# Optimization experiments

Measured on AMD Instinct MI355X. Metric: run time of the kernel, lower is better.

The kernel has to match this reference:

```python
import jax, jax.numpy as jnp
import numpy as np

M, K, N, E = 8192, 1024, 1024, 8  # total tokens, in-dim, out-dim, experts/segments


def setup_inputs() -> dict:
    key = jax.random.key(0)
    k1, k2, k3 = jax.random.split(key, 3)
    a = jax.random.normal(k1, (M, K), dtype=jnp.float32)
    b = jax.random.normal(k2, (E, N, K), dtype=jnp.float32) * 0.02  # column-major per-expert weights
    c = jnp.zeros((M, N), dtype=jnp.float32)
    inner = jnp.sort(jax.random.randint(k3, (E - 1,), 0, M, dtype=jnp.int32))
    seg_indptr = jnp.concatenate([
        jnp.zeros((1,), jnp.int32), inner, jnp.full((1,), M, jnp.int32)
    ])  # [E+1], monotone, covers [0, M)
    weight_indices = jnp.arange(E, dtype=jnp.int32)
    return {
        "a": a, "b": b, "c": c,
        "batch_size": E, "weight_column_major": 1,
        "seg_indptr": seg_indptr, "weight_indices": weight_indices,
    }


def reference(a, b, c, batch_size, weight_column_major, seg_indptr, weight_indices):
    # Grouped GEMM: for each contiguous segment s of rows [seg_indptr[s], seg_indptr[s+1]),
    # c[rows] = a[rows] @ b[weight_indices[s]].T  (b is [E, N, K], column-major weights).
    assert weight_column_major
    rows = jnp.arange(a.shape[0])[:, None]  # [M, 1]
    out = c
    for s in range(batch_size):  # fixed small loop over experts/segments
        b_e = jnp.take(b, weight_indices[s], axis=0)  # [N, K]
        seg_out = a @ b_e.T                            # [M, N]
        mask = (rows >= seg_indptr[s]) & (rows < seg_indptr[s + 1])
        out = jnp.where(mask, seg_out, out)
    return out
```

## Files before the change

kernel.cpp:

```cpp
#include <hip/hip_runtime.h>
#include <hip/hip_bf16.h>

#define MDIM 8192
#define KDIM 1024
#define NDIM 1024
#define NEXP 8
#define BM 128
#define BN 128
#define BK 32
#define LDSS 40

typedef __attribute__((ext_vector_type(8))) short bf16x8;
typedef __attribute__((ext_vector_type(4))) float floatx4;

static __device__ __forceinline__ unsigned short f2b(float f) {
    unsigned int u = __float_as_uint(f);
    return (unsigned short)((u + 0x7fffu + ((u >> 16) & 1u)) >> 16);
}

static __device__ __forceinline__ void cvt_store4(unsigned short* dst, float4 v) {
    ushort4 u;
    u.x = f2b(v.x); u.y = f2b(v.y); u.z = f2b(v.z); u.w = f2b(v.w);
    *reinterpret_cast<ushort4*>(dst) = u;
}

__global__ __launch_bounds__(256, 2)
void grouped_gemm_bf16(const float* __restrict__ a,
                       const float* __restrict__ b,
                       const int* __restrict__ seg_indptr,
                       const int* __restrict__ widx,
                       float* __restrict__ c)
{
    __shared__ unsigned short As[BM * LDSS];
    __shared__ unsigned short Bs[BN * LDSS];

    const int NTN = NDIM / BN;
    int rem = (int)blockIdx.x;
    int s = -1, m0 = 0, seg_end = 0, n0 = 0;
    for (int i = 0; i < NEXP; ++i) {
        int ps = seg_indptr[i], pe = seg_indptr[i + 1];
        int nt = ((pe - ps + BM - 1) / BM) * NTN;
        if (rem < nt) {
            s = i; m0 = ps + (rem / NTN) * BM; n0 = (rem % NTN) * BN; seg_end = pe;
            break;
        }
        rem -= nt;
    }
    if (s < 0) return;

    const float* __restrict__ be = b + (size_t)widx[s] * (size_t)(NDIM * KDIM);

    const int tid = (int)threadIdx.x;
    const int r0 = tid >> 3;
    const int kc = (tid & 7) * 4;

    int arow[4];
#pragma unroll
    for (int u = 0; u < 4; ++u) {
        int r = m0 + r0 + 32 * u;
        arow[u] = r < MDIM ? r : MDIM - 1;
    }

    const int lane = tid & 63;
    const int wave = tid >> 6;
    const int wm = (wave & 1) * 64;
    const int wn = (wave >> 1) * 64;
    const int fr = lane & 15;
    const int quad = lane >> 4;

    floatx4 acc[4][4] = {};

    float4 av[4], bv[4];
#pragma unroll
    for (int u = 0; u < 4; ++u) {
        av[u] = *reinterpret_cast<const float4*>(a + (size_t)arow[u] * KDIM + kc);
        bv[u] = *reinterpret_cast<const float4*>(be + (size_t)(n0 + r0 + 32 * u) * KDIM + kc);
    }

    for (int k0 = 0; k0 < KDIM; k0 += BK) {
        __syncthreads();
#pragma unroll
        for (int u = 0; u < 4; ++u) {
            cvt_store4(&As[(r0 + 32 * u) * LDSS + kc], av[u]);
            cvt_store4(&Bs[(r0 + 32 * u) * LDSS + kc], bv[u]);
        }
        const int kn = (k0 + BK < KDIM) ? (k0 + BK) : 0;
#pragma unroll
        for (int u = 0; u < 4; ++u) {
            av[u] = *reinterpret_cast<const float4*>(a + (size_t)arow[u] * KDIM + kn + kc);
            bv[u] = *reinterpret_cast<const float4*>(be + (size_t)(n0 + r0 + 32 * u) * KDIM + kn + kc);
        }
        __syncthreads();

        bf16x8 af[4], bf[4];
#pragma unroll
        for (int mi = 0; mi < 4; ++mi)
            af[mi] = *reinterpret_cast<const bf16x8*>(&As[(wm + mi * 16 + fr) * LDSS + quad * 8]);
#pragma unroll
        for (int ni = 0; ni < 4; ++ni)
            bf[ni] = *reinterpret_cast<const bf16x8*>(&Bs[(wn + ni * 16 + fr) * LDSS + quad * 8]);
#pragma unroll
        for (int mi = 0; mi < 4; ++mi)
#pragma unroll
            for (int ni = 0; ni < 4; ++ni)
                acc[mi][ni] = __builtin_amdgcn_mfma_f32_16x16x32_bf16(af[mi], bf[ni], acc[mi][ni], 0, 0, 0);
    }

#pragma unroll
    for (int mi = 0; mi < 4; ++mi) {
        const int rbase = m0 + wm + mi * 16 + quad * 4;
#pragma unroll
        for (int ni = 0; ni < 4; ++ni) {
            const int col = n0 + wn + ni * 16 + fr;
#pragma unroll
            for (int j = 0; j < 4; ++j) {
                const int row = rbase + j;
                if (row < seg_end)
                    c[(size_t)row * NDIM + col] = acc[mi][ni][j];
            }
        }
    }
}

extern "C" void kernel_launch(void* const* d_in, const int* in_sizes, int n_in,
                              void* d_out, int out_size, void* d_ws, size_t ws_size,
                              hipStream_t stream) {
    const float* a          = (const float*)d_in[0];
    const float* b          = (const float*)d_in[1];
    const int*   seg_indptr = (const int*)d_in[5];
    const int*   widx       = (const int*)d_in[6];
    float*       out        = (float*)d_out;

    dim3 grid(568), block(256);
    hipLaunchKernelGGL(grouped_gemm_bf16, grid, block, 0, stream,
                       a, b, seg_indptr, widx, out);
}
```

Baseline: 174.2 us.

## Pre-convert inputs to bf16 in workspace and stream tiles via global_load_lds

Adds a separate conversion kernel that casts A and all expert weights to bf16 into the workspace. The GEMM then reads half-width data and copies tiles straight into LDS with global_load_lds, removing per-tile in-register conversion and the register staging round trip. In exchange it pays an extra full read and write pass over A and B plus a second launch. It also drops the register prefetch and LDS padding, which can expose load latency and bank conflicts. The old fused kernel is kept as a fallback when the workspace is too small.

```diff
diff --git a/kernel.cpp b/kernel.cpp
--- a/kernel.cpp
+++ b/kernel.cpp
@@ -1,5 +1,6 @@
 #include <hip/hip_runtime.h>
 #include <hip/hip_bf16.h>
+#include <stdint.h>
 
 #define MDIM 8192
 #define KDIM 1024
@@ -12,27 +13,43 @@
 
 typedef __attribute__((ext_vector_type(8))) short bf16x8;
 typedef __attribute__((ext_vector_type(4))) float floatx4;
+typedef __attribute__((ext_vector_type(8))) unsigned short ushort8;
 
 static __device__ __forceinline__ unsigned short f2b(float f) {
     unsigned int u = __float_as_uint(f);
     return (unsigned short)((u + 0x7fffu + ((u >> 16) & 1u)) >> 16);
 }
 
-static __device__ __forceinline__ void cvt_store4(unsigned short* dst, float4 v) {
-    ushort4 u;
-    u.x = f2b(v.x); u.y = f2b(v.y); u.z = f2b(v.z); u.w = f2b(v.w);
-    *reinterpret_cast<ushort4*>(dst) = u;
-}
+__global__ __launch_bounds__(256)
+void cvt_bf16(const float* __restrict__ a, const float* __restrict__ b,
+              unsigned short* __restrict__ wa, unsigned short* __restrict__ wb)
+{
+    const long t  = (long)blockIdx.x * 256 + threadIdx.x;
+    const long NA = (long)MDIM * KDIM / 8;
+    const float* src; unsigned short* dst; long v;
+    if (t < NA) { src = a; dst = wa; v = t; }
+    else        { src = b; dst = wb; v = t - NA; }
+    const float4 lo = ((const float4*)src)[2 * v];
+    const float4 hi = ((const float4*)src)[2 * v + 1];
+    ushort8 o;
+    o[0] = f2b(lo.x); o[1] = f2b(lo.y); o[2] = f2b(lo.z); o[3] = f2b(lo.w);
+    o[4] = f2b(hi.x); o[5] = f2b(hi.y); o[6] = f2b(hi.z); o[7] = f2b(hi.w);
+    ((ushort8*)dst)[v] = o;
+}
+
+#define GLDS(gp, lp) __builtin_amdgcn_global_load_lds(                        \
+    (const __attribute__((address_space(1))) unsigned int*)(gp),              \
+    (__attribute__((address_space(3))) unsigned int*)(lp), 16, 0, 0)
 
 __global__ __launch_bounds__(256, 2)
-void grouped_gemm_bf16(const float* __restrict__ a,
-                       const float* __restrict__ b,
-                       const int* __restrict__ seg_indptr,
-                       const int* __restrict__ widx,
-                       float* __restrict__ c)
+void grouped_gemm_ws(const unsigned short* __restrict__ A,
+                     const unsigned short* __restrict__ B,
+                     const int* __restrict__ seg_indptr,
+                     const int* __restrict__ widx,
+                     float* __restrict__ c)
 {
-    __shared__ unsigned short As[BM * LDSS];
-    __shared__ unsigned short Bs[BN * LDSS];
+    __shared__ unsigned short As[BM * BK];
+    __shared__ unsigned short Bs[BN * BK];
 
     const int NTN = NDIM / BN;
     int rem = (int)blockIdx.x;
@@ -40,49 +57,122 @@
     for (int i = 0; i < NEXP; ++i) {
         int ps = seg_indptr[i], pe = seg_indptr[i + 1];
         int nt = ((pe - ps + BM - 1) / BM) * NTN;
-        if (rem < nt) {
-            s = i; m0 = ps + (rem / NTN) * BM; n0 = (rem % NTN) * BN; seg_end = pe;
-            break;
-        }
+        if (rem < nt) { s = i; m0 = ps + (rem / NTN) * BM; n0 = (rem % NTN) * BN; seg_end = pe; break; }
         rem -= nt;
     }
     if (s < 0) return;
 
+    const unsigned short* __restrict__ be = B + (size_t)widx[s] * (size_t)(NDIM * KDIM);
+
+    const int tid  = (int)threadIdx.x;
+    const int wave = tid >> 6;
+    const int lane = tid & 63;
+    const int srow = tid >> 2;
+    const int skc  = (tid & 3) * 8;
+    int arow0 = m0 + srow;       if (arow0 >= MDIM) arow0 = MDIM - 1;
+    int arow1 = m0 + 64 + srow;  if (arow1 >= MDIM) arow1 = MDIM - 1;
+    const int brow0 = n0 + srow, brow1 = n0 + 64 + srow;
+    const int ldsoff = wave * 16 * BK;
+
+    const int wm = (wave & 1) * 64;
+    const int wn = (wave >> 1) * 64;
+    const int fr = lane & 15;
+    const int quad = lane >> 4;
+
+    floatx4 acc[4][4] = {};
+
+    const unsigned short* aptr0 = A  + (size_t)arow0 * KDIM + skc;
+    const unsigned short* aptr1 = A  + (size_t)arow1 * KDIM + skc;
+    const unsigned short* bptr0 = be + (size_t)brow0 * KDIM + skc;
+    const unsigned short* bptr1 = be + (size_t)brow1 * KDIM + skc;
+
+    for (int k0 = 0; k0 < KDIM; k0 += BK) {
+        GLDS(aptr0 + k0, &As[ldsoff]);
+        GLDS(aptr1 + k0, &As[64 * BK + ldsoff]);
+        GLDS(bptr0 + k0, &Bs[ldsoff]);
+        GLDS(bptr1 + k0, &Bs[64 * BK + ldsoff]);
+        __syncthreads();
+
+        bf16x8 af[4], bf[4];
+#pragma unroll
+        for (int mi = 0; mi < 4; ++mi)
+            af[mi] = *reinterpret_cast<const bf16x8*>(&As[(wm + mi * 16 + fr) * BK + quad * 8]);
+#pragma unroll
+        for (int ni = 0; ni < 4; ++ni)
+            bf[ni] = *reinterpret_cast<const bf16x8*>(&Bs[(wn + ni * 16 + fr) * BK + quad * 8]);
+#pragma unroll
+        for (int mi = 0; mi < 4; ++mi)
+#pragma unroll
+            for (int ni = 0; ni < 4; ++ni)
+                acc[mi][ni] = __builtin_amdgcn_mfma_f32_16x16x32_bf16(af[mi], bf[ni], acc[mi][ni], 0, 0, 0);
+        __syncthreads();
+    }
+
+#pragma unroll
+    for (int mi = 0; mi < 4; ++mi) {
+        const int rbase = m0 + wm + mi * 16 + quad * 4;
+#pragma unroll
+        for (int ni = 0; ni < 4; ++ni) {
+            const int col = n0 + wn + ni * 16 + fr;
+#pragma unroll
+            for (int j = 0; j < 4; ++j) {
+                const int row = rbase + j;
+                if (row < seg_end)
+                    c[(size_t)row * NDIM + col] = acc[mi][ni][j];
+            }
+        }
+    }
+}
+
+__global__ __launch_bounds__(256, 2)
+void grouped_gemm_fused(const float* __restrict__ a, const float* __restrict__ b,
+                        const int* __restrict__ seg_indptr, const int* __restrict__ widx,
+                        float* __restrict__ c)
+{
+    __shared__ unsigned short As[BM * LDSS];
+    __shared__ unsigned short Bs[BN * LDSS];
+    const int NTN = NDIM / BN;
+    int rem = (int)blockIdx.x;
+    int s = -1, m0 = 0, seg_end = 0, n0 = 0;
+    for (int i = 0; i < NEXP; ++i) {
+        int ps = seg_indptr[i], pe = seg_indptr[i + 1];
+        int nt = ((pe - ps + BM - 1) / BM) * NTN;
+        if (rem < nt) { s = i; m0 = ps + (rem / NTN) * BM; n0 = (rem % NTN) * BN; seg_end = pe; break; }
+        rem -= nt;
+    }
+    if (s < 0) return;
     const float* __restrict__ be = b + (size_t)widx[s] * (size_t)(NDIM * KDIM);
-
     const int tid = (int)threadIdx.x;
     const int r0 = tid >> 3;
     const int kc = (tid & 7) * 4;
-
     int arow[4];
 #pragma unroll
     for (int u = 0; u < 4; ++u) {
         int r = m0 + r0 + 32 * u;
         arow[u] = r < MDIM ? r : MDIM - 1;
     }
-
     const int lane = tid & 63;
     const int wave = tid >> 6;
     const int wm = (wave & 1) * 64;
     const int wn = (wave >> 1) * 64;
     const int fr = lane & 15;
     const int quad = lane >> 4;
-
     floatx4 acc[4][4] = {};
-
     float4 av[4], bv[4];
 #pragma unroll
     for (int u = 0; u < 4; ++u) {
         av[u] = *reinterpret_cast<const float4*>(a + (size_t)arow[u] * KDIM + kc);
         bv[u] = *reinterpret_cast<const float4*>(be + (size_t)(n0 + r0 + 32 * u) * KDIM + kc);
     }
-
     for (int k0 = 0; k0 < KDIM; k0 += BK) {
         __syncthreads();
 #pragma unroll
         for (int u = 0; u < 4; ++u) {
-            cvt_store4(&As[(r0 + 32 * u) * LDSS + kc], av[u]);
-            cvt_store4(&Bs[(r0 + 32 * u) * LDSS + kc], bv[u]);
+            ushort4 ua, ub;
+            ua.x = f2b(av[u].x); ua.y = f2b(av[u].y); ua.z = f2b(av[u].z); ua.w = f2b(av[u].w);
+            ub.x = f2b(bv[u].x); ub.y = f2b(bv[u].y); ub.z = f2b(bv[u].z); ub.w = f2b(bv[u].w);
+            *reinterpret_cast<ushort4*>(&As[(r0 + 32 * u) * LDSS + kc]) = ua;
+            *reinterpret_cast<ushort4*>(&Bs[(r0 + 32 * u) * LDSS + kc]) = ub;
         }
         const int kn = (k0 + BK < KDIM) ? (k0 + BK) : 0;
 #pragma unroll
@@ -91,7 +181,6 @@
             bv[u] = *reinterpret_cast<const float4*>(be + (size_t)(n0 + r0 + 32 * u) * KDIM + kn + kc);
         }
         __syncthreads();
-
         bf16x8 af[4], bf[4];
 #pragma unroll
         for (int mi = 0; mi < 4; ++mi)
@@ -105,7 +194,6 @@
             for (int ni = 0; ni < 4; ++ni)
                 acc[mi][ni] = __builtin_amdgcn_mfma_f32_16x16x32_bf16(af[mi], bf[ni], acc[mi][ni], 0, 0, 0);
     }
-
 #pragma unroll
     for (int mi = 0; mi < 4; ++mi) {
         const int rbase = m0 + wm + mi * 16 + quad * 4;
@@ -131,7 +219,15 @@
     const int*   widx       = (const int*)d_in[6];
     float*       out        = (float*)d_out;
 
-    dim3 grid(568), block(256);
-    hipLaunchKernelGGL(grouped_gemm_bf16, grid, block, 0, stream,
-                       a, b, seg_indptr, widx, out);
-}
+    const size_t need = (size_t)(MDIM + NEXP * NDIM) * KDIM * sizeof(unsigned short);
+    if (ws_size >= need) {
+        unsigned short* wa = (unsigned short*)d_ws;
+        unsigned short* wb = wa + (size_t)MDIM * KDIM;
+        hipLaunchKernelGGL(cvt_bf16, dim3(8192), dim3(256), 0, stream, a, b, wa, wb);
+        hipLaunchKernelGGL(grouped_gemm_ws, dim3(568), dim3(256), 0, stream,
+                           wa, wb, seg_indptr, widx, out);
+    } else {
+        hipLaunchKernelGGL(grouped_gemm_fused, dim3(568), dim3(256), 0, stream,
+                           a, b, seg_indptr, widx, out);
+    }
+}
```

Result: faster. 168.0 us (-3.5%).

## Stage fp32 tiles via direct global-to-LDS loads with swizzle and double buffering

Applied to the files above, without the earlier changes.

Replaces register-staged fp32 loads with bf16 conversion before the LDS store by async global_load_lds of raw fp32 tiles into double-buffered LDS. A XOR swizzle avoids bank conflicts, and the bf16 packing moves to fragment-read time using the packed convert builtin when available. The block index is remapped across the 8 groups of the grid, likely for L2 locality. This removes the VGPR staging and conversion from the load path, but doubles LDS footprint and reads fp32 from LDS, which may cost occupancy and LDS bandwidth.

```diff
diff --git a/kernel.cpp b/kernel.cpp
--- a/kernel.cpp
+++ b/kernel.cpp
@@ -1,5 +1,6 @@
 #include <hip/hip_runtime.h>
 #include <hip/hip_bf16.h>
+#include <stdint.h>
 
 #define MDIM 8192
 #define KDIM 1024
@@ -8,102 +9,131 @@
 #define BM 128
 #define BN 128
 #define BK 32
-#define LDSS 40
 
 typedef __attribute__((ext_vector_type(8))) short bf16x8;
 typedef __attribute__((ext_vector_type(4))) float floatx4;
 
+#if __has_builtin(__builtin_amdgcn_cvt_pk_bf16_f32)
+typedef __attribute__((ext_vector_type(2))) __bf16 bf16x2v;
+static __device__ __forceinline__ int cvt2(float x, float y) {
+    bf16x2v r = __builtin_amdgcn_cvt_pk_bf16_f32(x, y);
+    return __builtin_bit_cast(int, r);
+}
+#else
 static __device__ __forceinline__ unsigned short f2b(float f) {
     unsigned int u = __float_as_uint(f);
     return (unsigned short)((u + 0x7fffu + ((u >> 16) & 1u)) >> 16);
 }
+static __device__ __forceinline__ int cvt2(float x, float y) {
+    return (int)f2b(x) | ((int)f2b(y) << 16);
+}
+#endif
 
-static __device__ __forceinline__ void cvt_store4(unsigned short* dst, float4 v) {
-    ushort4 u;
-    u.x = f2b(v.x); u.y = f2b(v.y); u.z = f2b(v.z); u.w = f2b(v.w);
-    *reinterpret_cast<ushort4*>(dst) = u;
+static __device__ __forceinline__ bf16x8 pack8(float4 a, float4 b) {
+    int4 r;
+    r.x = cvt2(a.x, a.y);
+    r.y = cvt2(a.z, a.w);
+    r.z = cvt2(b.x, b.y);
+    r.w = cvt2(b.z, b.w);
+    return __builtin_bit_cast(bf16x8, r);
 }
 
+#define GLDS(gp, lp) __builtin_amdgcn_global_load_lds(                        \
+    (const __attribute__((address_space(1))) unsigned int*)(gp),              \
+    (__attribute__((address_space(3))) unsigned int*)(lp), 16, 0, 0)
+
 __global__ __launch_bounds__(256, 2)
-void grouped_gemm_bf16(const float* __restrict__ a,
-                       const float* __restrict__ b,
-                       const int* __restrict__ seg_indptr,
-                       const int* __restrict__ widx,
-                       float* __restrict__ c)
+void grouped_gemm_f32(const float* __restrict__ A,
+                      const float* __restrict__ B,
+                      const int* __restrict__ seg_indptr,
+                      const int* __restrict__ widx,
+                      float* __restrict__ c)
 {
-    __shared__ unsigned short As[BM * LDSS];
-    __shared__ unsigned short Bs[BN * LDSS];
+    __shared__ float As0[BM * BK], As1[BM * BK];
+    __shared__ float Bs0[BN * BK], Bs1[BN * BK];
+
+    const int bid = ((int)blockIdx.x & 7) * 71 + ((int)blockIdx.x >> 3);
 
     const int NTN = NDIM / BN;
-    int rem = (int)blockIdx.x;
+    int rem = bid;
     int s = -1, m0 = 0, seg_end = 0, n0 = 0;
     for (int i = 0; i < NEXP; ++i) {
         int ps = seg_indptr[i], pe = seg_indptr[i + 1];
         int nt = ((pe - ps + BM - 1) / BM) * NTN;
-        if (rem < nt) {
-            s = i; m0 = ps + (rem / NTN) * BM; n0 = (rem % NTN) * BN; seg_end = pe;
-            break;
-        }
+        if (rem < nt) { s = i; m0 = ps + (rem / NTN) * BM; n0 = (rem % NTN) * BN; seg_end = pe; break; }
         rem -= nt;
     }
     if (s < 0) return;
 
-    const float* __restrict__ be = b + (size_t)widx[s] * (size_t)(NDIM * KDIM);
+    const float* __restrict__ be = B + (size_t)widx[s] * (size_t)(NDIM * KDIM);
 
-    const int tid = (int)threadIdx.x;
-    const int r0 = tid >> 3;
-    const int kc = (tid & 7) * 4;
+    const int tid  = (int)threadIdx.x;
+    const int wave = tid >> 6;
+    const int lane = tid & 63;
 
-    int arow[4];
+    const int srow = tid >> 3;
+    const int gch  = ((tid & 7) ^ (srow & 7)) * 4;
+    const float* ap[4];
+    const float* bp[4];
 #pragma unroll
-    for (int u = 0; u < 4; ++u) {
-        int r = m0 + r0 + 32 * u;
-        arow[u] = r < MDIM ? r : MDIM - 1;
+    for (int j = 0; j < 4; ++j) {
+        int ra = m0 + j * 32 + srow; if (ra >= MDIM) ra = MDIM - 1;
+        ap[j] = A  + (size_t)ra * KDIM + gch;
+        bp[j] = be + (size_t)(n0 + j * 32 + srow) * KDIM + gch;
     }
+    const int ldso = wave * 256;
 
-    const int lane = tid & 63;
-    const int wave = tid >> 6;
     const int wm = (wave & 1) * 64;
     const int wn = (wave >> 1) * 64;
-    const int fr = lane & 15;
+    const int fr   = lane & 15;
     const int quad = lane >> 4;
+    const int p0 = ((2 * quad) ^ (fr & 7)) * 4;
+    const int p1 = ((2 * quad + 1) ^ (fr & 7)) * 4;
 
     floatx4 acc[4][4] = {};
 
-    float4 av[4], bv[4];
-#pragma unroll
-    for (int u = 0; u < 4; ++u) {
-        av[u] = *reinterpret_cast<const float4*>(a + (size_t)arow[u] * KDIM + kc);
-        bv[u] = *reinterpret_cast<const float4*>(be + (size_t)(n0 + r0 + 32 * u) * KDIM + kc);
-    }
+#define STAGE(AS, BS, kk)                                                     \
+    do {                                                                      \
+        _Pragma("unroll")                                                     \
+        for (int j = 0; j < 4; ++j) {                                         \
+            GLDS(ap[j] + (kk), &AS[j * 1024 + ldso]);                         \
+            GLDS(bp[j] + (kk), &BS[j * 1024 + ldso]);                         \
+        }                                                                     \
+    } while (0)
 
-    for (int k0 = 0; k0 < KDIM; k0 += BK) {
+#define COMPUTE(AS, BS)                                                       \
+    do {                                                                      \
+        bf16x8 af[4], bf[4];                                                  \
+        _Pragma("unroll")                                                     \
+        for (int mi = 0; mi < 4; ++mi) {                                      \
+            const int base = (wm + mi * 16 + fr) * BK;                        \
+            af[mi] = pack8(*reinterpret_cast<const float4*>(&AS[base + p0]),  \
+                           *reinterpret_cast<const float4*>(&AS[base + p1])); \
+        }                                                                     \
+        _Pragma("unroll")                                                     \
+        for (int ni = 0; ni < 4; ++ni) {                                      \
+            const int base = (wn + ni * 16 + fr) * BK;                        \
+            bf[ni] = pack8(*reinterpret_cast<const float4*>(&BS[base + p0]),  \
+                           *reinterpret_cast<const float4*>(&BS[base + p1])); \
+        }                                                                     \
+        _Pragma("unroll")                                                     \
+        for (int mi = 0; mi < 4; ++mi)                                        \
+            _Pragma("unroll")                                                 \
+            for (int ni = 0; ni < 4; ++ni)                                    \
+                acc[mi][ni] = __builtin_amdgcn_mfma_f32_16x16x32_bf16(        \
+                    af[mi], bf[ni], acc[mi][ni], 0, 0, 0);                    \
+    } while (0)
+
+    STAGE(As0, Bs0, 0);
+#pragma unroll 1
+    for (int ii = 0; ii < 16; ++ii) {
+        const int i0 = ii * 2;
         __syncthreads();
-#pragma unroll
-        for (int u = 0; u < 4; ++u) {
-            cvt_store4(&As[(r0 + 32 * u) * LDSS + kc], av[u]);
-            cvt_store4(&Bs[(r0 + 32 * u) * LDSS + kc], bv[u]);
-        }
-        const int kn = (k0 + BK < KDIM) ? (k0 + BK) : 0;
-#pragma unroll
-        for (int u = 0; u < 4; ++u) {
-            av[u] = *reinterpret_cast<const float4*>(a + (size_t)arow[u] * KDIM + kn + kc);
-            bv[u] = *reinterpret_cast<const float4*>(be + (size_t)(n0 + r0 + 32 * u) * KDIM + kn + kc);
-        }
+        STAGE(As1, Bs1, (i0 + 1) * BK);
+        COMPUTE(As0, Bs0);
         __syncthreads();
-
-        bf16x8 af[4], bf[4];
-#pragma unroll
-        for (int mi = 0; mi < 4; ++mi)
-            af[mi] = *reinterpret_cast<const bf16x8*>(&As[(wm + mi * 16 + fr) * LDSS + quad * 8]);
-#pragma unroll
-        for (int ni = 0; ni < 4; ++ni)
-            bf[ni] = *reinterpret_cast<const bf16x8*>(&Bs[(wn + ni * 16 + fr) * LDSS + quad * 8]);
-#pragma unroll
-        for (int mi = 0; mi < 4; ++mi)
-#pragma unroll
-            for (int ni = 0; ni < 4; ++ni)
-                acc[mi][ni] = __builtin_amdgcn_mfma_f32_16x16x32_bf16(af[mi], bf[ni], acc[mi][ni], 0, 0, 0);
+        if (i0 + 2 < 32) STAGE(As0, Bs0, (i0 + 2) * BK);
+        COMPUTE(As1, Bs1);
     }
 
 #pragma unroll
@@ -120,6 +150,8 @@
             }
         }
     }
+#undef STAGE
+#undef COMPUTE
 }
 
 extern "C" void kernel_launch(void* const* d_in, const int* in_sizes, int n_in,
@@ -131,7 +163,6 @@
     const int*   widx       = (const int*)d_in[6];
     float*       out        = (float*)d_out;
 
-    dim3 grid(568), block(256);
-    hipLaunchKernelGGL(grouped_gemm_bf16, grid, block, 0, stream,
+    hipLaunchKernelGGL(grouped_gemm_f32, dim3(568), dim3(256), 0, stream,
                        a, b, seg_indptr, widx, out);
 }
```

Result: slower. 193.8 us (+11.2%).

## Pre-convert inputs to bf16 MFMA fragment layout and drop LDS staging

Applied to the files above, without the earlier changes.

Adds a pre-pass kernel that converts A and all expert weights from fp32 to bf16 and stores them in a workspace, already arranged in per-lane MFMA fragment order. The GEMM kernel then loads fragments straight from global memory into registers with double buffering, with no LDS and no barriers. It also aligns tile starts to 16 rows, masks rows on both segment ends, and swizzles block order. The aim is to halve the bytes the GEMM reads and remove per-tile conversion and synchronisation, at the cost of an extra pass over about 32 MB of fp32 input and more global load traffic per wave, since tiles no longer share operands through LDS.

```diff
diff --git a/kernel.cpp b/kernel.cpp
--- a/kernel.cpp
+++ b/kernel.cpp
@@ -1,109 +1,104 @@
 #include <hip/hip_runtime.h>
 #include <hip/hip_bf16.h>
+#include <stdint.h>
 
 #define MDIM 8192
 #define KDIM 1024
 #define NDIM 1024
 #define NEXP 8
-#define BM 128
-#define BN 128
-#define BK 32
-#define LDSS 40
 
 typedef __attribute__((ext_vector_type(8))) short bf16x8;
 typedef __attribute__((ext_vector_type(4))) float floatx4;
+typedef __attribute__((ext_vector_type(8))) unsigned short ushort8;
 
 static __device__ __forceinline__ unsigned short f2b(float f) {
     unsigned int u = __float_as_uint(f);
     return (unsigned short)((u + 0x7fffu + ((u >> 16) & 1u)) >> 16);
 }
 
-static __device__ __forceinline__ void cvt_store4(unsigned short* dst, float4 v) {
-    ushort4 u;
-    u.x = f2b(v.x); u.y = f2b(v.y); u.z = f2b(v.z); u.w = f2b(v.w);
-    *reinterpret_cast<ushort4*>(dst) = u;
+__global__ __launch_bounds__(256)
+void cvt_frag(const float* __restrict__ a, const float* __restrict__ b,
+              unsigned short* __restrict__ w)
+{
+    const int t = (int)blockIdx.x * 256 + (int)threadIdx.x;
+    const int f = t >> 6, l = t & 63;
+    const int vrow = ((f >> 5) << 4) + (l & 15);
+    const int kk   = ((f & 31) << 5) + ((l >> 4) << 3);
+    const float* __restrict__ src = (vrow < MDIM)
+        ? a + (size_t)vrow * KDIM + kk
+        : b + (size_t)(vrow - MDIM) * KDIM + kk;
+    const float4 lo = *reinterpret_cast<const float4*>(src);
+    const float4 hi = *reinterpret_cast<const float4*>(src + 4);
+    ushort8 o;
+    o[0] = f2b(lo.x); o[1] = f2b(lo.y); o[2] = f2b(lo.z); o[3] = f2b(lo.w);
+    o[4] = f2b(hi.x); o[5] = f2b(hi.y); o[6] = f2b(hi.z); o[7] = f2b(hi.w);
+    *reinterpret_cast<ushort8*>(w + (size_t)f * 512 + l * 8) = o;
 }
 
-__global__ __launch_bounds__(256, 2)
-void grouped_gemm_bf16(const float* __restrict__ a,
-                       const float* __restrict__ b,
+__global__ __launch_bounds__(256, 3)
+void grouped_gemm_frag(const unsigned short* __restrict__ W,
                        const int* __restrict__ seg_indptr,
                        const int* __restrict__ widx,
                        float* __restrict__ c)
 {
-    __shared__ unsigned short As[BM * LDSS];
-    __shared__ unsigned short Bs[BN * LDSS];
+    const int bid = ((int)blockIdx.x & 7) * 72 + ((int)blockIdx.x >> 3);
 
-    const int NTN = NDIM / BN;
-    int rem = (int)blockIdx.x;
-    int s = -1, m0 = 0, seg_end = 0, n0 = 0;
+    int rem = bid;
+    int s = -1, m0 = 0, n0 = 0, seg_s = 0, seg_e = 0;
     for (int i = 0; i < NEXP; ++i) {
         int ps = seg_indptr[i], pe = seg_indptr[i + 1];
-        int nt = ((pe - ps + BM - 1) / BM) * NTN;
-        if (rem < nt) {
-            s = i; m0 = ps + (rem / NTN) * BM; n0 = (rem % NTN) * BN; seg_end = pe;
-            break;
-        }
+        int start = ps & ~15;
+        int nt = ((pe - start + 127) >> 7) * 8;
+        if (rem < nt) { s = i; m0 = start + (rem >> 3) * 128; n0 = (rem & 7) * 128; seg_s = ps; seg_e = pe; break; }
         rem -= nt;
     }
     if (s < 0) return;
 
-    const float* __restrict__ be = b + (size_t)widx[s] * (size_t)(NDIM * KDIM);
+    const int wave = (int)threadIdx.x >> 6;
+    const int lane = (int)threadIdx.x & 63;
+    const int wm = (wave & 1) * 64;
+    const int wn = (wave >> 1) * 64;
+    const int fr   = lane & 15;
+    const int quad = lane >> 4;
 
-    const int tid = (int)threadIdx.x;
-    const int r0 = tid >> 3;
-    const int kc = (tid & 7) * 4;
+    const size_t ia  = (size_t)((m0 + wm) >> 4);
+    const size_t ibv = (size_t)((MDIM + widx[s] * NDIM + n0 + wn) >> 4);
+    const unsigned short* __restrict__ ap = W + ia  * 16384 + lane * 8;
+    const unsigned short* __restrict__ bp = W + ibv * 16384 + lane * 8;
 
-    int arow[4];
+    floatx4 acc[4][4] = {};
+    bf16x8 af[2][4], bf[2][4];
+
 #pragma unroll
-    for (int u = 0; u < 4; ++u) {
-        int r = m0 + r0 + 32 * u;
-        arow[u] = r < MDIM ? r : MDIM - 1;
+    for (int t = 0; t < 4; ++t) {
+        af[0][t] = *reinterpret_cast<const bf16x8*>(ap + t * 16384);
+        bf[0][t] = *reinterpret_cast<const bf16x8*>(bp + t * 16384);
     }
 
-    const int lane = tid & 63;
-    const int wave = tid >> 6;
-    const int wm = (wave & 1) * 64;
-    const int wn = (wave >> 1) * 64;
-    const int fr = lane & 15;
-    const int quad = lane >> 4;
-
-    floatx4 acc[4][4] = {};
-
-    float4 av[4], bv[4];
+#pragma unroll 1
+    for (int j = 0; j < 32; j += 2) {
 #pragma unroll
-    for (int u = 0; u < 4; ++u) {
-        av[u] = *reinterpret_cast<const float4*>(a + (size_t)arow[u] * KDIM + kc);
-        bv[u] = *reinterpret_cast<const float4*>(be + (size_t)(n0 + r0 + 32 * u) * KDIM + kc);
-    }
-
-    for (int k0 = 0; k0 < KDIM; k0 += BK) {
-        __syncthreads();
-#pragma unroll
-        for (int u = 0; u < 4; ++u) {
-            cvt_store4(&As[(r0 + 32 * u) * LDSS + kc], av[u]);
-            cvt_store4(&Bs[(r0 + 32 * u) * LDSS + kc], bv[u]);
+        for (int t = 0; t < 4; ++t) {
+            af[1][t] = *reinterpret_cast<const bf16x8*>(ap + t * 16384 + (j + 1) * 512);
+            bf[1][t] = *reinterpret_cast<const bf16x8*>(bp + t * 16384 + (j + 1) * 512);
         }
-        const int kn = (k0 + BK < KDIM) ? (k0 + BK) : 0;
-#pragma unroll
-        for (int u = 0; u < 4; ++u) {
-            av[u] = *reinterpret_cast<const float4*>(a + (size_t)arow[u] * KDIM + kn + kc);
-            bv[u] = *reinterpret_cast<const float4*>(be + (size_t)(n0 + r0 + 32 * u) * KDIM + kn + kc);
-        }
-        __syncthreads();
-
-        bf16x8 af[4], bf[4];
-#pragma unroll
-        for (int mi = 0; mi < 4; ++mi)
-            af[mi] = *reinterpret_cast<const bf16x8*>(&As[(wm + mi * 16 + fr) * LDSS + quad * 8]);
-#pragma unroll
-        for (int ni = 0; ni < 4; ++ni)
-            bf[ni] = *reinterpret_cast<const bf16x8*>(&Bs[(wn + ni * 16 + fr) * LDSS + quad * 8]);
 #pragma unroll
         for (int mi = 0; mi < 4; ++mi)
 #pragma unroll
             for (int ni = 0; ni < 4; ++ni)
-                acc[mi][ni] = __builtin_amdgcn_mfma_f32_16x16x32_bf16(af[mi], bf[ni], acc[mi][ni], 0, 0, 0);
+                acc[mi][ni] = __builtin_amdgcn_mfma_f32_16x16x32_bf16(af[0][mi], bf[0][ni], acc[mi][ni], 0, 0, 0);
+
+        const int jn = (j + 2 < 32) ? (j + 2) : 0;
+#pragma unroll
+        for (int t = 0; t < 4; ++t) {
+            af[0][t] = *reinterpret_cast<const bf16x8*>(ap + t * 16384 + jn * 512);
+            bf[0][t] = *reinterpret_cast<const bf16x8*>(bp + t * 16384 + jn * 512);
+        }
+#pragma unroll
+        for (int mi = 0; mi < 4; ++mi)
+#pragma unroll
+            for (int ni = 0; ni < 4; ++ni)
+                acc[mi][ni] = __builtin_amdgcn_mfma_f32_16x16x32_bf16(af[1][mi], bf[1][ni], acc[mi][ni], 0, 0, 0);
     }
 
 #pragma unroll
@@ -115,7 +110,7 @@
 #pragma unroll
             for (int j = 0; j < 4; ++j) {
                 const int row = rbase + j;
-                if (row < seg_end)
+                if (row >= seg_s && row < seg_e)
                     c[(size_t)row * NDIM + col] = acc[mi][ni][j];
             }
         }
@@ -131,7 +126,9 @@
     const int*   widx       = (const int*)d_in[6];
     float*       out        = (float*)d_out;
 
-    dim3 grid(568), block(256);
-    hipLaunchKernelGGL(grouped_gemm_bf16, grid, block, 0, stream,
-                       a, b, seg_indptr, widx, out);
+    unsigned short* w = (unsigned short*)d_ws;
+
+    hipLaunchKernelGGL(cvt_frag, dim3(8192), dim3(256), 0, stream, a, b, w);
+    hipLaunchKernelGGL(grouped_gemm_frag, dim3(576), dim3(256), 0, stream,
+                       w, seg_indptr, widx, out);
 }
```

Measured after the change: 167.4 us. 1.04x faster.
